# Optimization experiments

Hardware: AMD Instinct MI355X
Metric: run time of the kernel (lower is better)

Reference implementation:

```python
import jax, jax.numpy as jnp
import numpy as np

L, D, H, F, V, S, M, B = 6, 256, 8, 1024, 3000, 512, 1024, 16
DH = D // H


def setup_inputs() -> dict:
    key = jax.random.key(0)
    ks = jax.random.split(key, 16)
    p = lambda k, shape: jax.random.normal(k, shape, jnp.float32) * 0.02
    return {
        "encoded": jax.random.normal(ks[0], (B, M, D), jnp.float32),
        "seq": jax.random.randint(ks[1], (B, S), 0, V),
        "input_embed": p(ks[2], (V, D)),            # shared with output projection
        "pos_embed": p(ks[3], (S, D)),
        "output_bias": jnp.zeros((V,), jnp.float32),
        "sa_qkv": p(ks[4], (L, 3, D, D)),            # self-attn Wq/Wk/Wv per layer
        "sa_o": p(ks[5], (L, D, D)),
        "ca_q": p(ks[6], (L, D, D)),                 # cross-attn Wq
        "ca_kv": p(ks[7], (L, 2, D, D)),             # cross-attn Wk/Wv
        "ca_o": p(ks[8], (L, D, D)),
        "ffn_w1": p(ks[9], (L, D, F)),
        "ffn_b1": jnp.zeros((L, F), jnp.float32),
        "ffn_w2": p(ks[10], (L, F, D)),
        "ffn_b2": jnp.zeros((L, D), jnp.float32),
        "ln_g": jnp.ones((L, 3, D), jnp.float32),    # 3 post-norms per layer
        "ln_b": jnp.zeros((L, 3, D), jnp.float32),
        "fin_g": jnp.ones((D,), jnp.float32),        # self.norm
        "fin_b": jnp.zeros((D,), jnp.float32),
    }


def _ln(x, g, b, eps=1e-5):
    mu = x.mean(-1, keepdims=True)
    var = ((x - mu) ** 2).mean(-1, keepdims=True)
    return (x - mu) * jax.lax.rsqrt(var + eps) * g + b


def _heads(t):  # [b, n, D] -> [b, n, H, DH]
    return t.reshape(t.shape[0], t.shape[1], H, DH)


def _attn(q_in, kv_in, Wq, Wk, Wv, Wo, mask):
    scale = 1.0 / np.sqrt(DH)
    q = _heads(q_in @ Wq)
    k = _heads(kv_in @ Wk)
    v = _heads(kv_in @ Wv)
    s = jnp.einsum("bqhd,bkhd->bhqk", q, k) * scale
    if mask is not None:
        s = jnp.where(mask, s, jnp.float32(-1e9))
    a = jax.nn.softmax(s, axis=-1)
    o = jnp.einsum("bhqk,bkhd->bqhd", a, v).reshape(q_in.shape)
    return o @ Wo


def reference(encoded, seq, input_embed, pos_embed, output_bias, sa_qkv, sa_o,
              ca_q, ca_kv, ca_o, ffn_w1, ffn_b1, ffn_w2, ffn_b2, ln_g, ln_b,
              fin_g, fin_b):
    seq_len = seq.shape[1]
    x = input_embed[seq] + pos_embed[:seq_len]           # [B, S, D]
    causal = jnp.tril(jnp.ones((seq_len, seq_len), bool))  # self_mask = tril ones
    for i in range(L):
        x = _ln(x + _attn(x, x, sa_qkv[i, 0], sa_qkv[i, 1], sa_qkv[i, 2],
                          sa_o[i], causal), ln_g[i, 0], ln_b[i, 0])
        x = _ln(x + _attn(x, encoded, ca_q[i], ca_kv[i, 0], ca_kv[i, 1],
                          ca_o[i], None), ln_g[i, 1], ln_b[i, 1])
        h = jax.nn.relu(x @ ffn_w1[i] + ffn_b1[i]) @ ffn_w2[i] + ffn_b2[i]
        x = _ln(x + h, ln_g[i, 2], ln_b[i, 2])
    x = _ln(x, fin_g, fin_b)                              # self.norm in decoder()
    return x @ input_embed.T + output_bias                # shared output_embed
```

## Files before the change

### kernel.cpp

```cpp
#include <hip/hip_runtime.h>
#include <hip/hip_bf16.h>

#define DD 256
#define HH 8
#define DH 32
#define SS 512
#define MM 1024
#define BB 16
#define FF 1024
#define LL 6
#define VV 3000

typedef __bf16 bf16x8 __attribute__((ext_vector_type(8)));
typedef float  f32x4  __attribute__((ext_vector_type(4)));

#define W_QKV0 0u
#define W_SAO0 1179648u
#define W_CAQ0 1572864u
#define W_CKV0 1966080u
#define W_CAO0 2752512u
#define W_W10  3145728u
#define W_W20  4718592u
#define W_EMB0 6291456u
#define W_TOT  7061504u

__device__ __forceinline__ float ldx(const void* p, size_t i, int bf) {
    if (bf) return __bfloat162float(((const __hip_bfloat16*)p)[i]);
    return ((const float*)p)[i];
}

__device__ __forceinline__ void split1(float v, __bf16& h, __bf16& l) {
    h = (__bf16)v;
    l = (__bf16)(v - (float)h);
}

__device__ __forceinline__ int swzi(int row, int c) {
    return row * 64 + ((c ^ (row & 7)) << 3);
}

__global__ void detect_k(const unsigned int* __restrict__ w, int* __restrict__ flag) {
    int t = threadIdx.x;
    unsigned int v = w[t];
    int ok = 1;
#pragma unroll
    for (int h = 0; h < 2; ++h) {
        unsigned int hw = (v >> (16 * h)) & 0xFFFFu;
        unsigned int e = (hw >> 7) & 0xFFu;
        if (!((e >= 90u && e <= 140u) || (hw & 0x7FFFu) == 0u)) ok = 0;
    }
    __shared__ int allok;
    if (t == 0) allok = 1;
    __syncthreads();
    if (!ok) atomicAnd(&allok, 0);
    __syncthreads();
    if (t == 0) *flag = allok;
}

__global__ __launch_bounds__(256)
void wsplit_k(const void* __restrict__ sa_qkv, const void* __restrict__ sa_o,
              const void* __restrict__ ca_q, const void* __restrict__ ca_kv,
              const void* __restrict__ ca_o, const void* __restrict__ w1,
              const void* __restrict__ w2,
              __bf16* __restrict__ Wh, __bf16* __restrict__ Wl,
              const int* __restrict__ flagp) {
    int bfw = *flagp;
    __shared__ float tile[64][65];
    int blk = blockIdx.x;
    int l = blk >> 8, r = blk & 255;
    const void* src; size_t soff, doff; int K_, N_, ti;
    if (r < 48)       { src = sa_qkv; int j = r >> 4; ti = r & 15;
                        soff = (size_t)(l * 3 + j) * 65536; doff = W_QKV0 + soff; K_ = 256; N_ = 256; }
    else if (r < 64)  { src = sa_o;  ti = r - 48;  soff = (size_t)l * 65536; doff = W_SAO0 + soff; K_ = 256; N_ = 256; }
    else if (r < 80)  { src = ca_q;  ti = r - 64;  soff = (size_t)l * 65536; doff = W_CAQ0 + soff; K_ = 256; N_ = 256; }
    else if (r < 112) { src = ca_kv; int j = (r - 80) >> 4; ti = (r - 80) & 15;
                        soff = (size_t)(l * 2 + j) * 65536; doff = W_CKV0 + soff; K_ = 256; N_ = 256; }
    else if (r < 128) { src = ca_o;  ti = r - 112; soff = (size_t)l * 65536; doff = W_CAO0 + soff; K_ = 256; N_ = 256; }
    else if (r < 192) { src = w1;    ti = r - 128; soff = (size_t)l * 262144; doff = W_W10 + soff; K_ = 256; N_ = 1024; }
    else              { src = w2;    ti = r - 192; soff = (size_t)l * 262144; doff = W_W20 + soff; K_ = 1024; N_ = 256; }
    int ntil = N_ >> 6;
    int kt = ti / ntil, nt = ti % ntil;
    int k0 = kt * 64, n0 = nt * 64;
    int t = threadIdx.x;
#pragma unroll
    for (int rr = 0; rr < 16; ++rr) {
        int kk = rr * 4 + (t >> 6), nn = t & 63;
        tile[kk][nn] = ldx(src, soff + (size_t)(k0 + kk) * N_ + n0 + nn, bfw);
    }
    __syncthreads();
#pragma unroll
    for (int rr = 0; rr < 16; ++rr) {
        int nn = rr * 4 + (t >> 6), kk = t & 63;
        float v = tile[kk][nn];
        size_t o = doff + (size_t)(n0 + nn) * K_ + k0 + kk;
        split1(v, Wh[o], Wl[o]);
    }
}

__global__ void embsplit_k(const void* __restrict__ emb,
                           __bf16* __restrict__ Wh, __bf16* __restrict__ Wl,
                           const int* __restrict__ flagp) {
    int bfw = *flagp;
    int row = blockIdx.x;
    int d = threadIdx.x;
    float v = (row < VV) ? ldx(emb, (size_t)row * DD + d, bfw) : 0.f;
    size_t o = W_EMB0 + (size_t)row * DD + d;
    split1(v, Wh[o], Wl[o]);
}

__global__ void embed_k(const int* __restrict__ seq,
                        const void* __restrict__ emb,
                        const void* __restrict__ pos,
                        float* __restrict__ x,
                        __bf16* __restrict__ xh,
                        __bf16* __restrict__ xl,
                        const int* __restrict__ flagp) {
    int bf = *flagp;
    int row = blockIdx.x;
    int d = threadIdx.x;
    int s = row & (SS - 1);
    int b = row >> 9;
    int tok = seq[b * SS + s];
    float v = ldx(emb, (size_t)tok * DD + d, bf) + ldx(pos, (size_t)s * DD + d, bf);
    size_t idx = (size_t)row * DD + d;
    x[idx] = v;
    split1(v, xh[idx], xl[idx]);
}

template <int AMODE, int OUTMODE>
__global__ __launch_bounds__(128, 3)
void gemm_mfma_k(const void* __restrict__ A, const void* __restrict__ Al_,
                 const __bf16* __restrict__ Wh, const __bf16* __restrict__ Wl, size_t boff,
                 const char* __restrict__ biasbase, size_t biasoff, int hasbias,
                 void* __restrict__ C, void* __restrict__ C2,
                 int M, int N, int K, int relu,
                 int nsplit, size_t cstride,
                 const int* __restrict__ flagp) {
    int bfw = *flagp;
    const __bf16* Bh_g = Wh + boff;
    const __bf16* Bl_g = Wl + boff;
    int t = threadIdx.x;
    int lane = t & 63;
    int wv = t >> 6;

    int gx = gridDim.x;
    int nwg = gx * gridDim.y;
    int id = blockIdx.y * gx + blockIdx.x;
    int q = nwg >> 3, r = nwg & 7;
    int xcd = id & 7, sub = id >> 3;
    int nid = (xcd < r ? xcd * (q + 1) : r * (q + 1) + (xcd - r) * q) + sub;
    int nB0 = (nid % gx) * 64;
    int m0  = (nid / gx) * 64;

    int n0 = nB0;
    int ldc = N;
    float* Cf = (float*)C;
    __bf16* Ch = (__bf16*)C;
    __bf16* Cl2 = (__bf16*)C2;
    if (nsplit) {
        int mat = n0 / nsplit;
        n0 -= mat * nsplit;
        Cf  += (size_t)mat * cstride;
        Ch  += (size_t)mat * cstride;
        Cl2 += (size_t)mat * cstride;
        ldc = nsplit;
    }

    __shared__ __align__(16) __bf16 Ahl[4096];
    __shared__ __align__(16) __bf16 Bhl[4096];

    f32x4 acc[2][4] = {};
    int fr = lane & 15;
    int fg = lane >> 4;
    int t_alo = !(AMODE == 1 && bfw);
    int t_blo = !bfw;

    int srow = t >> 1;
    int h2 = t & 1;

    bf16x8 pah[2], pal[2], pbh[2], pbl[2];

    auto loadA = [&](int k0) {
        size_t g = (size_t)(m0 + srow) * K + k0 + h2 * 16;
        if (AMODE == 2) {
            pah[0] = *(const bf16x8*)((const __bf16*)A + g);
            pah[1] = *(const bf16x8*)((const __bf16*)A + g + 8);
            pal[0] = *(const bf16x8*)((const __bf16*)Al_ + g);
            pal[1] = *(const bf16x8*)((const __bf16*)Al_ + g + 8);
        } else if (bfw) {
            pah[0] = *(const bf16x8*)((const __hip_bfloat16*)A + g);
            pah[1] = *(const bf16x8*)((const __hip_bfloat16*)A + g + 8);
        } else {
#pragma unroll
            for (int c = 0; c < 2; ++c) {
                float4 f1 = *(const float4*)((const float*)A + g + c * 8);
                float4 f2 = *(const float4*)((const float*)A + g + c * 8 + 4);
                float vv[8] = {f1.x, f1.y, f1.z, f1.w, f2.x, f2.y, f2.z, f2.w};
                bf16x8 hv, lv;
#pragma unroll
                for (int e = 0; e < 8; ++e) { __bf16 h, l; split1(vv[e], h, l); hv[e] = h; lv[e] = l; }
                pah[c] = hv; pal[c] = lv;
            }
        }
    };
    auto loadB = [&](int k0) {
        size_t g = (size_t)(nB0 + srow) * K + k0 + h2 * 16;
        pbh[0] = *(const bf16x8*)(Bh_g + g);
        pbh[1] = *(const bf16x8*)(Bh_g + g + 8);
        pbl[0] = *(const bf16x8*)(Bl_g + g);
        pbl[1] = *(const bf16x8*)(Bl_g + g + 8);
    };
    auto writeLDS = [&]() {
#pragma unroll
        for (int j = 0; j < 2; ++j) {
            int ch = h2 * 2 + j;
            *(bf16x8*)&Ahl[swzi(srow, ch)] = pah[j];
            *(bf16x8*)&Bhl[swzi(srow, ch)] = pbh[j];
            *(bf16x8*)&Bhl[swzi(srow, 4 + ch)] = pbl[j];
            if (!(AMODE == 1 && bfw))
                *(bf16x8*)&Ahl[swzi(srow, 4 + ch)] = pal[j];
        }
    };

    loadA(0); loadB(0);
    for (int k0 = 0; k0 < K; k0 += 32) {
        writeLDS();
        __syncthreads();
        if (k0 + 32 < K) { loadA(k0 + 32); loadB(k0 + 32); }

        bf16x8 afh[2], afl[2], bgh[4], bgl[4];
#pragma unroll
        for (int f = 0; f < 2; ++f) {
            int row = wv * 32 + f * 16 + fr;
            afh[f] = *(const bf16x8*)&Ahl[swzi(row, fg)];
            afl[f] = *(const bf16x8*)&Ahl[swzi(row, 4 + fg)];
        }
#pragma unroll
        for (int f = 0; f < 4; ++f) {
            int row = f * 16 + fr;
            bgh[f] = *(const bf16x8*)&Bhl[swzi(row, fg)];
            bgl[f] = *(const bf16x8*)&Bhl[swzi(row, 4 + fg)];
        }
#pragma unroll
        for (int mf = 0; mf < 2; ++mf)
#pragma unroll
            for (int nf = 0; nf < 4; ++nf) {
                acc[mf][nf] = __builtin_amdgcn_mfma_f32_16x16x32_bf16(afh[mf], bgh[nf], acc[mf][nf], 0, 0, 0);
                if (t_alo)
                    acc[mf][nf] = __builtin_amdgcn_mfma_f32_16x16x32_bf16(afl[mf], bgh[nf], acc[mf][nf], 0, 0, 0);
                if (t_blo)
                    acc[mf][nf] = __builtin_amdgcn_mfma_f32_16x16x32_bf16(afh[mf], bgl[nf], acc[mf][nf], 0, 0, 0);
            }
        __syncthreads();
    }

    const char* biasp = biasbase + biasoff * (bfw ? 2 : 4);
#pragma unroll
    for (int mf = 0; mf < 2; ++mf)
#pragma unroll
        for (int nf = 0; nf < 4; ++nf)
#pragma unroll
            for (int r2 = 0; r2 < 4; ++r2) {
                int row = m0 + wv * 32 + mf * 16 + fg * 4 + r2;
                int col = n0 + nf * 16 + fr;
                float v = acc[mf][nf][r2];
                if (OUTMODE == 2) {
                    if (col < N) {
                        v += ldx(biasp, col, bfw);
                        size_t oi = (size_t)row * N + col;
                        if (bfw) ((__hip_bfloat16*)C)[oi] = __float2bfloat16(v);
                        else     ((float*)C)[oi] = v;
                    }
                } else {
                    if (hasbias) v += ldx(biasp, col, bfw);
                    if (relu) v = fmaxf(v, 0.f);
                    size_t oi = (size_t)row * ldc + col;
                    if (OUTMODE == 1) {
                        __bf16 h, l; split1(v, h, l);
                        Ch[oi]  = h;
                        Cl2[oi] = l;
                    } else if (OUTMODE == 3) {
                        Ch[oi] = (__bf16)v;
                    } else {
                        Cf[oi] = v;
                    }
                }
            }
}

template <int CAUSAL>
__global__ __launch_bounds__(256)
void attn_mfma_k(const __bf16* __restrict__ Qg,
                 const __bf16* __restrict__ Kg,
                 const __bf16* __restrict__ Vg,
                 __bf16* __restrict__ Oh, __bf16* __restrict__ Ol,
                 int Sk) {
    __shared__ __align__(16) __bf16 Ks[64][40];
    __shared__ __align__(16) __bf16 Vt[32][66];
    __shared__ __align__(16) __bf16 Ps[4][16][72];

    int t = threadIdx.x;
    int lane = t & 63;
    int w = t >> 6;
    int l15 = lane & 15;
    int g = lane >> 4;

    int blk = blockIdx.x;
    int qt = blk & 7;
    int h  = (blk >> 3) & (HH - 1);
    int b  = blk >> 6;
    int q0 = qt * 64;

    const float scale = 0.17677669529663689f;

    bf16x8 q_;
    {
        size_t qi = ((size_t)(b * SS + q0 + w * 16 + l15)) * DD + h * 32 + g * 8;
        bf16x8 q8 = *(const bf16x8*)(Qg + qi);
#pragma unroll
        for (int j = 0; j < 8; ++j) q_[j] = (__bf16)((float)q8[j] * scale);
    }

    f32x4 oacc[2] = {};
    float m_r[4] = {-1e30f, -1e30f, -1e30f, -1e30f};
    float l_r[4] = {0.f, 0.f, 0.f, 0.f};

    int ntiles = CAUSAL ? (qt + 1) : (Sk >> 6);

    for (int tt = 0; tt < ntiles; ++tt) {
        int j0 = tt * 64;
        {
            int row = t >> 2, db = (t & 3) * 8;
            size_t gi = ((size_t)(b * Sk + j0 + row)) * DD + h * 32 + db;
            *(bf16x8*)&Ks[row][db] = *(const bf16x8*)(Kg + gi);
            bf16x8 v8 = *(const bf16x8*)(Vg + gi);
#pragma unroll
            for (int j = 0; j < 8; ++j) Vt[db + j][row] = v8[j];
        }
        __syncthreads();

        f32x4 s[4] = {};
#pragma unroll
        for (int kt = 0; kt < 4; ++kt) {
            bf16x8 kb = *(const bf16x8*)&Ks[kt * 16 + l15][g * 8];
            s[kt] = __builtin_amdgcn_mfma_f32_16x16x32_bf16(q_, kb, s[kt], 0, 0, 0);
        }

        if (CAUSAL && tt == ntiles - 1) {
            int qa_ = q0 + w * 16 + g * 4;
#pragma unroll
            for (int kt = 0; kt < 4; ++kt)
#pragma unroll
                for (int r = 0; r < 4; ++r)
                    if (j0 + kt * 16 + l15 > qa_ + r) s[kt][r] = -1e30f;
        }

        float al_r[4];
#pragma unroll
        for (int r = 0; r < 4; ++r) {
            float mx = fmaxf(fmaxf(s[0][r], s[1][r]), fmaxf(s[2][r], s[3][r]));
#pragma unroll
            for (int off = 1; off < 16; off <<= 1) mx = fmaxf(mx, __shfl_xor(mx, off));
            float mnew = fmaxf(m_r[r], mx);
            al_r[r] = __expf(m_r[r] - mnew);
            float ps = 0.f;
#pragma unroll
            for (int kt = 0; kt < 4; ++kt) {
                float p = __expf(s[kt][r] - mnew);
                s[kt][r] = p;
                ps += p;
            }
#pragma unroll
            for (int off = 1; off < 16; off <<= 1) ps += __shfl_xor(ps, off);
            l_r[r] = l_r[r] * al_r[r] + ps;
            m_r[r] = mnew;
        }
#pragma unroll
        for (int dt = 0; dt < 2; ++dt)
#pragma unroll
            for (int r = 0; r < 4; ++r) oacc[dt][r] *= al_r[r];
#pragma unroll
        for (int kt = 0; kt < 4; ++kt)
#pragma unroll
            for (int r = 0; r < 4; ++r)
                Ps[w][g * 4 + r][kt * 16 + l15] = (__bf16)s[kt][r];
        __syncthreads();

#pragma unroll
        for (int kc = 0; kc < 2; ++kc) {
            bf16x8 pa = *(const bf16x8*)&Ps[w][l15][kc * 32 + g * 8];
#pragma unroll
            for (int dt = 0; dt < 2; ++dt) {
                bf16x8 vb = *(const bf16x8*)&Vt[dt * 16 + l15][kc * 32 + g * 8];
                oacc[dt] = __builtin_amdgcn_mfma_f32_16x16x32_bf16(pa, vb, oacc[dt], 0, 0, 0);
            }
        }
        __syncthreads();
    }

    float inv[4];
#pragma unroll
    for (int r = 0; r < 4; ++r) inv[r] = 1.f / l_r[r];
#pragma unroll
    for (int dt = 0; dt < 2; ++dt)
#pragma unroll
        for (int r = 0; r < 4; ++r) {
            float v = oacc[dt][r] * inv[r];
            size_t oi = ((size_t)(b * SS + q0 + w * 16 + g * 4 + r)) * DD + h * 32 + dt * 16 + l15;
            __bf16 hh, ll; split1(v, hh, ll);
            Oh[oi] = hh;
            Ol[oi] = ll;
        }
}

__global__ void add_ln_k(float* __restrict__ x,
                         const float* __restrict__ hbuf,
                         __bf16* __restrict__ xh,
                         __bf16* __restrict__ xl,
                         const char* __restrict__ gbase, size_t goff,
                         const char* __restrict__ bbase, size_t boff,
                         const int* __restrict__ flagp) {
    int bf = *flagp;
    const void* g = gbase + goff * (bf ? 2 : 4);
    const void* bb = bbase + boff * (bf ? 2 : 4);
    int row = blockIdx.x;
    int d = threadIdx.x;
    float v = x[(size_t)row * DD + d];
    if (hbuf) v += hbuf[(size_t)row * DD + d];
    float s = v, s2 = v * v;
#pragma unroll
    for (int off = 32; off > 0; off >>= 1) {
        s += __shfl_down(s, off);
        s2 += __shfl_down(s2, off);
    }
    __shared__ float sh[8];
    int w = d >> 6;
    if ((d & 63) == 0) { sh[w] = s; sh[4 + w] = s2; }
    __syncthreads();
    if (d == 0) {
        sh[0] = sh[0] + sh[1] + sh[2] + sh[3];
        sh[4] = sh[4] + sh[5] + sh[6] + sh[7];
    }
    __syncthreads();
    float mu = sh[0] * (1.f / DD);
    float var = fmaxf(sh[4] * (1.f / DD) - mu * mu, 0.f);
    float inv = rsqrtf(var + 1e-5f);
    float o = (v - mu) * inv * ldx(g, d, bf) + ldx(bb, d, bf);
    size_t idx = (size_t)row * DD + d;
    x[idx] = o;
    split1(o, xh[idx], xl[idx]);
}

extern "C" void kernel_launch(void* const* d_in, const int* in_sizes, int n_in,
                              void* d_out, int out_size, void* d_ws, size_t ws_size,
                              hipStream_t stream) {
    const void* encoded     = d_in[0];
    const int*  seq         = (const int*)d_in[1];
    const void* input_embed = d_in[2];
    const void* pos_embed   = d_in[3];
    const void* output_bias = d_in[4];
    const void* sa_qkv      = d_in[5];
    const void* sa_o        = d_in[6];
    const void* ca_q        = d_in[7];
    const void* ca_kv       = d_in[8];
    const void* ca_o        = d_in[9];
    const void* ffn_w1      = d_in[10];
    const char* ffn_b1      = (const char*)d_in[11];
    const void* ffn_w2      = d_in[12];
    const char* ffn_b2      = (const char*)d_in[13];
    const char* ln_g        = (const char*)d_in[14];
    const char* ln_b        = (const char*)d_in[15];
    const char* fin_g       = (const char*)d_in[16];
    const char* fin_b       = (const char*)d_in[17];

    const size_t NTOK = (size_t)BB * SS;
    const size_t NENC = (size_t)BB * MM;

    char* p = (char*)d_ws;
    int*    flag = (int*)p;            p += 256;
    float*  x    = (float*)p;          p += NTOK * DD * 4;
    __bf16* xh   = (__bf16*)p;         p += NTOK * DD * 2;
    __bf16* xl   = (__bf16*)p;         p += NTOK * DD * 2;
    __bf16* SAh  = (__bf16*)p;         p += 3 * NTOK * DD * 2;
    __bf16* SAl  = (__bf16*)p;         p += 3 * NTOK * DD * 2;
    __bf16* CKh  = (__bf16*)p;         p += 2 * NENC * DD * 2;
    __bf16* CKl  = (__bf16*)p;         p += 2 * NENC * DD * 2;
    __bf16* Wh   = (__bf16*)p;         p += (size_t)W_TOT * 2;
    __bf16* Wl   = (__bf16*)p;         p += (size_t)W_TOT * 2;
    float*  Tb = (float*)(SAh + NTOK * DD);
    __bf16* Oh = xh;   __bf16* Ol = xl;
    __bf16* Hh = CKh;  __bf16* Hl = CKl;

    detect_k<<<1, 256, 0, stream>>>((const unsigned int*)input_embed, flag);
    wsplit_k<<<1536, 256, 0, stream>>>(sa_qkv, sa_o, ca_q, ca_kv, ca_o,
                                       ffn_w1, ffn_w2, Wh, Wl, flag);
    embsplit_k<<<3008, 256, 0, stream>>>(input_embed, Wh, Wl, flag);
    embed_k<<<NTOK, 256, 0, stream>>>(seq, input_embed, pos_embed, x, xh, xl, flag);

    dim3 blk(128);
    dim3 gQKV(12, 128);
    dim3 gP(4, 128);
    dim3 gCKV(8, 256);
    dim3 gW1(16, 128);
    dim3 gOut(47, 128);
    int attn_blocks = BB * HH * (SS / 64);

    for (int l = 0; l < LL; ++l) {
        size_t oQKV = W_QKV0 + (size_t)l * 3 * 65536;
        size_t oSAO = W_SAO0 + (size_t)l * 65536;
        size_t oCAQ = W_CAQ0 + (size_t)l * 65536;
        size_t oCKV = W_CKV0 + (size_t)l * 2 * 65536;
        size_t oCAO = W_CAO0 + (size_t)l * 65536;
        size_t oW1  = W_W10  + (size_t)l * 262144;
        size_t oW2  = W_W20  + (size_t)l * 262144;
        size_t oB1  = (size_t)l * FF;
        size_t oB2  = (size_t)l * DD;
        size_t oG   = (size_t)l * 3 * DD;

        gemm_mfma_k<2, 3><<<gQKV, blk, 0, stream>>>(xh, xl, Wh, Wl, oQKV,
            nullptr, 0, 0, SAh, nullptr, (int)NTOK, 3 * DD, DD, 0, DD, NTOK * DD, flag);
        attn_mfma_k<1><<<attn_blocks, 256, 0, stream>>>(SAh,
            SAh + NTOK * DD, SAh + 2 * NTOK * DD, Oh, Ol, SS);
        gemm_mfma_k<2, 0><<<gP, blk, 0, stream>>>(Oh, Ol, Wh, Wl, oSAO,
            nullptr, 0, 0, Tb, nullptr, (int)NTOK, DD, DD, 0, 0, 0, flag);
        add_ln_k<<<NTOK, 256, 0, stream>>>(x, Tb, xh, xl, ln_g, oG, ln_b, oG, flag);
        gemm_mfma_k<2, 3><<<gP, blk, 0, stream>>>(xh, xl, Wh, Wl, oCAQ,
            nullptr, 0, 0, SAh, nullptr, (int)NTOK, DD, DD, 0, 0, 0, flag);
        gemm_mfma_k<1, 3><<<gCKV, blk, 0, stream>>>(encoded, nullptr, Wh, Wl, oCKV,
            nullptr, 0, 0, CKh, nullptr, (int)NENC, 2 * DD, DD, 0, DD, NENC * DD, flag);
        attn_mfma_k<0><<<attn_blocks, 256, 0, stream>>>(SAh,
            CKh, CKh + NENC * DD, Oh, Ol, MM);
        gemm_mfma_k<2, 0><<<gP, blk, 0, stream>>>(Oh, Ol, Wh, Wl, oCAO,
            nullptr, 0, 0, Tb, nullptr, (int)NTOK, DD, DD, 0, 0, 0, flag);
        add_ln_k<<<NTOK, 256, 0, stream>>>(x, Tb, xh, xl, ln_g, oG + DD, ln_b, oG + DD, flag);
        gemm_mfma_k<2, 1><<<gW1, blk, 0, stream>>>(xh, xl, Wh, Wl, oW1,
            ffn_b1, oB1, 1, Hh, Hl, (int)NTOK, FF, DD, 1, 0, 0, flag);
        gemm_mfma_k<2, 0><<<gP, blk, 0, stream>>>(Hh, Hl, Wh, Wl, oW2,
            ffn_b2, oB2, 1, Tb, nullptr, (int)NTOK, DD, FF, 0, 0, 0, flag);
        add_ln_k<<<NTOK, 256, 0, stream>>>(x, Tb, xh, xl, ln_g, oG + 2 * DD, ln_b, oG + 2 * DD, flag);
    }
    add_ln_k<<<NTOK, 256, 0, stream>>>(x, nullptr, xh, xl, fin_g, 0, fin_b, 0, flag);
    gemm_mfma_k<2, 2><<<gOut, blk, 0, stream>>>(xh, xl, Wh, Wl, W_EMB0,
        (const char*)output_bias, 0, 1, d_out, nullptr, (int)NTOK, VV, DD, 0, 0, 0, flag);
}
```

Measured before the change: 1.896 ms.

## Drop weight low-part MFMAs for hidden GEMMs and halve M-tile on N=256 GEMMs

Adds template parameters so the GEMM kernel can skip the low-bf16 weight split (BSPL=0), removing one of three MFMAs and the Bl loads for every layer GEMM except the output projection. It also adds a 32-row M tile (MFR=1), used with a doubled grid for the N=256 projections, to raise block count and occupancy on those small GEMMs. This lowers weight precision to single bf16 for most GEMMs when fp32 weights are used, which may add error, and it trades per-block reuse for more parallelism.

```diff
diff --git a/kernel.cpp b/kernel.cpp
--- a/kernel.cpp
+++ b/kernel.cpp
@@ -126,7 +126,7 @@
     split1(v, xh[idx], xl[idx]);
 }
 
-template <int AMODE, int OUTMODE>
+template <int AMODE, int OUTMODE, int MFR, int BSPL>
 __global__ __launch_bounds__(128, 3)
 void gemm_mfma_k(const void* __restrict__ A, const void* __restrict__ Al_,
                  const __bf16* __restrict__ Wh, const __bf16* __restrict__ Wl, size_t boff,
@@ -135,6 +135,7 @@
                  int M, int N, int K, int relu,
                  int nsplit, size_t cstride,
                  const int* __restrict__ flagp) {
+    const int BM = 32 * MFR;
     int bfw = *flagp;
     const __bf16* Bh_g = Wh + boff;
     const __bf16* Bl_g = Wl + boff;
@@ -149,7 +150,7 @@
     int xcd = id & 7, sub = id >> 3;
     int nid = (xcd < r ? xcd * (q + 1) : r * (q + 1) + (xcd - r) * q) + sub;
     int nB0 = (nid % gx) * 64;
-    int m0  = (nid / gx) * 64;
+    int m0  = (nid / gx) * BM;
 
     int n0 = nB0;
     int ldc = N;
@@ -165,59 +166,61 @@
         ldc = nsplit;
     }
 
-    __shared__ __align__(16) __bf16 Ahl[4096];
+    __shared__ __align__(16) __bf16 Ahl[BM * 64];
     __shared__ __align__(16) __bf16 Bhl[4096];
 
-    f32x4 acc[2][4] = {};
+    f32x4 acc[MFR][4] = {};
     int fr = lane & 15;
     int fg = lane >> 4;
     int t_alo = !(AMODE == 1 && bfw);
-    int t_blo = !bfw;
-
-    int srow = t >> 1;
-    int h2 = t & 1;
+    int t_blo = BSPL && !bfw;
+
+    int arow = (MFR == 2) ? (t >> 1) : (t >> 2);
+    int ac0  = (MFR == 2) ? ((t & 1) * 2) : (t & 3);
+    int brow = t >> 1;
+    int bc0  = (t & 1) * 2;
 
     bf16x8 pah[2], pal[2], pbh[2], pbl[2];
 
     auto loadA = [&](int k0) {
-        size_t g = (size_t)(m0 + srow) * K + k0 + h2 * 16;
-        if (AMODE == 2) {
-            pah[0] = *(const bf16x8*)((const __bf16*)A + g);
-            pah[1] = *(const bf16x8*)((const __bf16*)A + g + 8);
-            pal[0] = *(const bf16x8*)((const __bf16*)Al_ + g);
-            pal[1] = *(const bf16x8*)((const __bf16*)Al_ + g + 8);
-        } else if (bfw) {
-            pah[0] = *(const bf16x8*)((const __hip_bfloat16*)A + g);
-            pah[1] = *(const bf16x8*)((const __hip_bfloat16*)A + g + 8);
-        } else {
-#pragma unroll
-            for (int c = 0; c < 2; ++c) {
-                float4 f1 = *(const float4*)((const float*)A + g + c * 8);
-                float4 f2 = *(const float4*)((const float*)A + g + c * 8 + 4);
+#pragma unroll
+        for (int j = 0; j < MFR; ++j) {
+            size_t g = (size_t)(m0 + arow) * K + k0 + (ac0 + j) * 8;
+            if (AMODE == 2) {
+                pah[j] = *(const bf16x8*)((const __bf16*)A + g);
+                pal[j] = *(const bf16x8*)((const __bf16*)Al_ + g);
+            } else if (bfw) {
+                pah[j] = *(const bf16x8*)((const __hip_bfloat16*)A + g);
+            } else {
+                float4 f1 = *(const float4*)((const float*)A + g);
+                float4 f2 = *(const float4*)((const float*)A + g + 4);
                 float vv[8] = {f1.x, f1.y, f1.z, f1.w, f2.x, f2.y, f2.z, f2.w};
                 bf16x8 hv, lv;
 #pragma unroll
                 for (int e = 0; e < 8; ++e) { __bf16 h, l; split1(vv[e], h, l); hv[e] = h; lv[e] = l; }
-                pah[c] = hv; pal[c] = lv;
+                pah[j] = hv; pal[j] = lv;
             }
         }
     };
     auto loadB = [&](int k0) {
-        size_t g = (size_t)(nB0 + srow) * K + k0 + h2 * 16;
-        pbh[0] = *(const bf16x8*)(Bh_g + g);
-        pbh[1] = *(const bf16x8*)(Bh_g + g + 8);
-        pbl[0] = *(const bf16x8*)(Bl_g + g);
-        pbl[1] = *(const bf16x8*)(Bl_g + g + 8);
+#pragma unroll
+        for (int j = 0; j < 2; ++j) {
+            size_t g = (size_t)(nB0 + brow) * K + k0 + (bc0 + j) * 8;
+            pbh[j] = *(const bf16x8*)(Bh_g + g);
+            if (BSPL) pbl[j] = *(const bf16x8*)(Bl_g + g);
+        }
     };
     auto writeLDS = [&]() {
 #pragma unroll
+        for (int j = 0; j < MFR; ++j) {
+            *(bf16x8*)&Ahl[swzi(arow, ac0 + j)] = pah[j];
+            if (!(AMODE == 1 && bfw))
+                *(bf16x8*)&Ahl[swzi(arow, 4 + ac0 + j)] = pal[j];
+        }
+#pragma unroll
         for (int j = 0; j < 2; ++j) {
-            int ch = h2 * 2 + j;
-            *(bf16x8*)&Ahl[swzi(srow, ch)] = pah[j];
-            *(bf16x8*)&Bhl[swzi(srow, ch)] = pbh[j];
-            *(bf16x8*)&Bhl[swzi(srow, 4 + ch)] = pbl[j];
-            if (!(AMODE == 1 && bfw))
-                *(bf16x8*)&Ahl[swzi(srow, 4 + ch)] = pal[j];
+            *(bf16x8*)&Bhl[swzi(brow, bc0 + j)] = pbh[j];
+            if (BSPL) *(bf16x8*)&Bhl[swzi(brow, 4 + bc0 + j)] = pbl[j];
         }
     };
 
@@ -227,10 +230,10 @@
         __syncthreads();
         if (k0 + 32 < K) { loadA(k0 + 32); loadB(k0 + 32); }
 
-        bf16x8 afh[2], afl[2], bgh[4], bgl[4];
-#pragma unroll
-        for (int f = 0; f < 2; ++f) {
-            int row = wv * 32 + f * 16 + fr;
+        bf16x8 afh[MFR], afl[MFR], bgh[4], bgl[4];
+#pragma unroll
+        for (int f = 0; f < MFR; ++f) {
+            int row = wv * (16 * MFR) + f * 16 + fr;
             afh[f] = *(const bf16x8*)&Ahl[swzi(row, fg)];
             afl[f] = *(const bf16x8*)&Ahl[swzi(row, 4 + fg)];
         }
@@ -238,16 +241,16 @@
         for (int f = 0; f < 4; ++f) {
             int row = f * 16 + fr;
             bgh[f] = *(const bf16x8*)&Bhl[swzi(row, fg)];
-            bgl[f] = *(const bf16x8*)&Bhl[swzi(row, 4 + fg)];
-        }
-#pragma unroll
-        for (int mf = 0; mf < 2; ++mf)
+            if (BSPL) bgl[f] = *(const bf16x8*)&Bhl[swzi(row, 4 + fg)];
+        }
+#pragma unroll
+        for (int mf = 0; mf < MFR; ++mf)
 #pragma unroll
             for (int nf = 0; nf < 4; ++nf) {
                 acc[mf][nf] = __builtin_amdgcn_mfma_f32_16x16x32_bf16(afh[mf], bgh[nf], acc[mf][nf], 0, 0, 0);
                 if (t_alo)
                     acc[mf][nf] = __builtin_amdgcn_mfma_f32_16x16x32_bf16(afl[mf], bgh[nf], acc[mf][nf], 0, 0, 0);
-                if (t_blo)
+                if (BSPL && t_blo)
                     acc[mf][nf] = __builtin_amdgcn_mfma_f32_16x16x32_bf16(afh[mf], bgl[nf], acc[mf][nf], 0, 0, 0);
             }
         __syncthreads();
@@ -255,12 +258,12 @@
 
     const char* biasp = biasbase + biasoff * (bfw ? 2 : 4);
 #pragma unroll
-    for (int mf = 0; mf < 2; ++mf)
+    for (int mf = 0; mf < MFR; ++mf)
 #pragma unroll
         for (int nf = 0; nf < 4; ++nf)
 #pragma unroll
             for (int r2 = 0; r2 < 4; ++r2) {
-                int row = m0 + wv * 32 + mf * 16 + fg * 4 + r2;
+                int row = m0 + wv * (16 * MFR) + mf * 16 + fg * 4 + r2;
                 int col = n0 + nf * 16 + fr;
                 float v = acc[mf][nf][r2];
                 if (OUTMODE == 2) {
@@ -498,7 +501,7 @@
 
     dim3 blk(128);
     dim3 gQKV(12, 128);
-    dim3 gP(4, 128);
+    dim3 gP(4, 256);
     dim3 gCKV(8, 256);
     dim3 gW1(16, 128);
     dim3 gOut(47, 128);
@@ -516,29 +519,29 @@
         size_t oB2  = (size_t)l * DD;
         size_t oG   = (size_t)l * 3 * DD;
 
-        gemm_mfma_k<2, 3><<<gQKV, blk, 0, stream>>>(xh, xl, Wh, Wl, oQKV,
+        gemm_mfma_k<2, 3, 2, 0><<<gQKV, blk, 0, stream>>>(xh, xl, Wh, Wl, oQKV,
             nullptr, 0, 0, SAh, nullptr, (int)NTOK, 3 * DD, DD, 0, DD, NTOK * DD, flag);
         attn_mfma_k<1><<<attn_blocks, 256, 0, stream>>>(SAh,
             SAh + NTOK * DD, SAh + 2 * NTOK * DD, Oh, Ol, SS);
-        gemm_mfma_k<2, 0><<<gP, blk, 0, stream>>>(Oh, Ol, Wh, Wl, oSAO,
+        gemm_mfma_k<2, 0, 1, 0><<<gP, blk, 0, stream>>>(Oh, Ol, Wh, Wl, oSAO,
             nullptr, 0, 0, Tb, nullptr, (int)NTOK, DD, DD, 0, 0, 0, flag);
         add_ln_k<<<NTOK, 256, 0, stream>>>(x, Tb, xh, xl, ln_g, oG, ln_b, oG, flag);
-        gemm_mfma_k<2, 3><<<gP, blk, 0, stream>>>(xh, xl, Wh, Wl, oCAQ,
+        gemm_mfma_k<2, 3, 1, 0><<<gP, blk, 0, stream>>>(xh, xl, Wh, Wl, oCAQ,
             nullptr, 0, 0, SAh, nullptr, (int)NTOK, DD, DD, 0, 0, 0, flag);
-        gemm_mfma_k<1, 3><<<gCKV, blk, 0, stream>>>(encoded, nullptr, Wh, Wl, oCKV,
+        gemm_mfma_k<1, 3, 2, 0><<<gCKV, blk, 0, stream>>>(encoded, nullptr, Wh, Wl, oCKV,
             nullptr, 0, 0, CKh, nullptr, (int)NENC, 2 * DD, DD, 0, DD, NENC * DD, flag);
         attn_mfma_k<0><<<attn_blocks, 256, 0, stream>>>(SAh,
             CKh, CKh + NENC * DD, Oh, Ol, MM);
-        gemm_mfma_k<2, 0><<<gP, blk, 0, stream>>>(Oh, Ol, Wh, Wl, oCAO,
+        gemm_mfma_k<2, 0, 1, 0><<<gP, blk, 0, stream>>>(Oh, Ol, Wh, Wl, oCAO,
             nullptr, 0, 0, Tb, nullptr, (int)NTOK, DD, DD, 0, 0, 0, flag);
         add_ln_k<<<NTOK, 256, 0, stream>>>(x, Tb, xh, xl, ln_g, oG + DD, ln_b, oG + DD, flag);
-        gemm_mfma_k<2, 1><<<gW1, blk, 0, stream>>>(xh, xl, Wh, Wl, oW1,
+        gemm_mfma_k<2, 1, 2, 0><<<gW1, blk, 0, stream>>>(xh, xl, Wh, Wl, oW1,
             ffn_b1, oB1, 1, Hh, Hl, (int)NTOK, FF, DD, 1, 0, 0, flag);
-        gemm_mfma_k<2, 0><<<gP, blk, 0, stream>>>(Hh, Hl, Wh, Wl, oW2,
+        gemm_mfma_k<2, 0, 1, 0><<<gP, blk, 0, stream>>>(Hh, Hl, Wh, Wl, oW2,
             ffn_b2, oB2, 1, Tb, nullptr, (int)NTOK, DD, FF, 0, 0, 0, flag);
         add_ln_k<<<NTOK, 256, 0, stream>>>(x, Tb, xh, xl, ln_g, oG + 2 * DD, ln_b, oG + 2 * DD, flag);
     }
     add_ln_k<<<NTOK, 256, 0, stream>>>(x, nullptr, xh, xl, fin_g, 0, fin_b, 0, flag);
-    gemm_mfma_k<2, 2><<<gOut, blk, 0, stream>>>(xh, xl, Wh, Wl, W_EMB0,
+    gemm_mfma_k<2, 2, 2, 1><<<gOut, blk, 0, stream>>>(xh, xl, Wh, Wl, W_EMB0,
         (const char*)output_bias, 0, 1, d_out, nullptr, (int)NTOK, VV, DD, 0, 0, 0, flag);
 }
```

New measurement: 1.711 ms. -9.7%, faster.
